# Performance work log

Hardware: AMD Instinct MI355X
Metric: run time of the kernel (lower is better)

The kernel has to match this reference:

```python
import jax, jax.numpy as jnp
import numpy as np

EPS = 1e-06


def euler_xyz_to_mat(e):
    # scipy Rotation.from_euler('xyz', [a,b,c]) is extrinsic: R = Rz(c) @ Ry(b) @ Rx(a)
    a, b, c = e[..., 0], e[..., 1], e[..., 2]
    sa, ca = jnp.sin(a), jnp.cos(a)
    sb, cb = jnp.sin(b), jnp.cos(b)
    sc, cc = jnp.sin(c), jnp.cos(c)
    r00 = cc * cb
    r01 = cc * sb * sa - sc * ca
    r02 = cc * sb * ca + sc * sa
    r10 = sc * cb
    r11 = sc * sb * sa + cc * ca
    r12 = sc * sb * ca - cc * sa
    r20 = -sb
    r21 = cb * sa
    r22 = cb * ca
    R = jnp.stack([r00, r01, r02, r10, r11, r12, r20, r21, r22], axis=-1)
    return R.reshape(e.shape[:-1] + (3, 3))


def to_transform(positions, orientations):
    # positions, orientations: [B, S, 3] -> poses [B, S, 4, 4]
    R = euler_xyz_to_mat(orientations)
    top = jnp.concatenate([R, positions[..., None]], axis=-1)  # [B,S,3,4]
    bottom = jnp.broadcast_to(
        jnp.array([0.0, 0.0, 0.0, 1.0], dtype=positions.dtype),
        positions.shape[:2] + (1, 4))
    return jnp.concatenate([top, bottom], axis=-2)


def odometry_to_track(poses):
    # cumulative left-product along seq: track[0]=I, track[i]=track[i-1] @ poses[:, i]
    B = poses.shape[0]
    eye = jnp.broadcast_to(jnp.eye(4, dtype=poses.dtype), (B, 1, 4, 4))
    shifted = jnp.concatenate([eye, poses[:, 1:]], axis=1)
    return jax.lax.associative_scan(
        lambda x, y: jnp.einsum('bsij,bsjk->bsik', x, y), shifted, axis=1)


def rotation_loss(rot1, rot2):
    # geodesic angle between rotations via trace of R1 @ R2^T
    R = jnp.einsum('bsij,bskj->bsik', rot1, rot2)
    cos = (R[:, :, 0, 0] + R[:, :, 1, 1] + R[:, :, 2, 2] - 1.0) / 2.0
    cos = jnp.clip(cos, -1.0 + EPS, 1.0 - EPS)
    return jnp.mean(jnp.arccos(cos))


def setup_inputs() -> dict:
    key = jax.random.key(0)
    k1, k2, k3 = jax.random.split(key, 3)
    B, S = 64, 4096
    return {
        'y_hat': jax.random.normal(k1, (B, S, 6), dtype=jnp.float32),
        'gt_positions': jax.random.normal(k2, (B, S, 3), dtype=jnp.float32),
        'gt_orientations': jax.random.normal(k3, (B, S, 3), dtype=jnp.float32),
    }


def reference(y_hat, gt_positions, gt_orientations):
    alphas = (1.0, 1.0)
    betas = (1.0, 1.0)
    gammas = (0.5, 0.5)

    pred_ori = y_hat[:, :, :3]
    pred_pos = y_hat[:, :, 3:]

    # ---- odometry loss ----
    mse_pos = jnp.mean((pred_pos - gt_positions) ** 2)
    mae_pos = jnp.mean(jnp.abs(pred_pos - gt_positions))
    pose_est = to_transform(pred_pos, pred_ori)
    pose_gt = to_transform(gt_positions, gt_orientations)
    odom_rot = rotation_loss(pose_est[:, :, :3, :3], pose_gt[:, :, :3, :3])
    odom_loss = alphas[0] * odom_rot + alphas[1] * (mse_pos + mae_pos)

    # ---- trajectory loss ----
    traj_gt = odometry_to_track(pose_gt)
    traj_est = odometry_to_track(pose_est)
    t_gt = traj_gt[:, :, :3, 3]
    t_est = traj_est[:, :, :3, 3]
    traj_mse = jnp.mean((t_est - t_gt) ** 2)
    traj_mae = jnp.mean(jnp.abs(t_est - t_gt))
    traj_rot = rotation_loss(traj_est[:, :, :3, :3], traj_gt[:, :, :3, :3])
    traj_loss = betas[0] * traj_rot + betas[1] * (traj_mse + traj_mae)

    return gammas[0] * odom_loss + gammas[1] * traj_loss
```

## Files before the change

kernel.cpp:

```cpp
#include <hip/hip_runtime.h>
#include <math.h>

#define NB 64
#define NS 4096
#define SEGS 8
#define TPB 256
#define CHUNK 2
#define STEPS (NS / SEGS)
#define NWAVES (TPB / 64)
#define NSEGB (NB * SEGS)
#define K3_TPB 512
#define K3_W (K3_TPB / 64)
#define FTPB 512

#define FB_T 512
#define FB_CHUNK (NS / FB_T)
#define FB_W (FB_T / 64)

struct Q {
  float w, x, y, z;
};
struct QT {
  Q q;
  float tx, ty, tz;
};

__device__ __forceinline__ Q qmul(const Q &a, const Q &b) {
  Q c;
  c.w = a.w * b.w - a.x * b.x - a.y * b.y - a.z * b.z;
  c.x = a.w * b.x + b.w * a.x + a.y * b.z - a.z * b.y;
  c.y = a.w * b.y + b.w * a.y + a.z * b.x - a.x * b.z;
  c.z = a.w * b.z + b.w * a.z + a.x * b.y - a.y * b.x;
  return c;
}

__device__ __forceinline__ Q qconj(const Q &q) {
  Q c;
  c.w = q.w;
  c.x = -q.x;
  c.y = -q.y;
  c.z = -q.z;
  return c;
}

__device__ __forceinline__ void qrot(const Q &q, float vx, float vy, float vz,
                                     float &ox, float &oy, float &oz) {
  const float tx = 2.f * (q.y * vz - q.z * vy);
  const float ty = 2.f * (q.z * vx - q.x * vz);
  const float tz = 2.f * (q.x * vy - q.y * vx);
  ox = vx + q.w * tx + (q.y * tz - q.z * ty);
  oy = vy + q.w * ty + (q.z * tx - q.x * tz);
  oz = vz + q.w * tz + (q.x * ty - q.y * tx);
}

__device__ __forceinline__ void qt_id(QT &x) {
  x.q.w = 1.f;
  x.q.x = x.q.y = x.q.z = 0.f;
  x.tx = x.ty = x.tz = 0.f;
}

__device__ __forceinline__ QT qt_mul(const QT &a, const QT &b) {
  QT c;
  c.q = qmul(a.q, b.q);
  float rx, ry, rz;
  qrot(a.q, b.tx, b.ty, b.tz, rx, ry, rz);
  c.tx = rx + a.tx;
  c.ty = ry + a.ty;
  c.tz = rz + a.tz;
  return c;
}

__device__ __forceinline__ QT qt_shfl_up(const QT &v, int delta) {
  QT y;
  y.q.w = __shfl_up(v.q.w, delta, 64);
  y.q.x = __shfl_up(v.q.x, delta, 64);
  y.q.y = __shfl_up(v.q.y, delta, 64);
  y.q.z = __shfl_up(v.q.z, delta, 64);
  y.tx = __shfl_up(v.tx, delta, 64);
  y.ty = __shfl_up(v.ty, delta, 64);
  y.tz = __shfl_up(v.tz, delta, 64);
  return y;
}

__device__ __forceinline__ float fast_acosf(float x) {
  const float ax = fabsf(x);
  float p = fmaf(ax, -0.0187293f, 0.0742610f);
  p = fmaf(p, ax, -0.2121144f);
  p = fmaf(p, ax, 1.5707288f);
  const float r = sqrtf(fmaxf(1.f - ax, 0.f)) * p;
  return (x >= 0.f) ? r : (3.14159274f - r);
}

__device__ __forceinline__ float angle_from_cos(float cosv) {
  cosv = fminf(fmaxf(cosv, -1.f + 1e-6f), 1.f - 1e-6f);
  return fast_acosf(cosv);
}

__device__ __forceinline__ Q euler_to_quat(float a, float b, float c) {
  float sa, ca, sb, cb, sc, cc;
  __sincosf(0.5f * a, &sa, &ca);
  __sincosf(0.5f * b, &sb, &cb);
  __sincosf(0.5f * c, &sc, &cc);
  Q q;
  q.w = cc * cb * ca + sc * sb * sa;
  q.x = cc * cb * sa - sc * sb * ca;
  q.y = cc * sb * ca + sc * cb * sa;
  q.z = sc * cb * ca - cc * sb * sa;
  return q;
}

__device__ __forceinline__ void block_reduce3_store(float v0, float v1,
                                                    float v2,
                                                    float *__restrict__ dst,
                                                    int lane, int wave,
                                                    int tid, int nwaves) {
#pragma unroll
  for (int o = 32; o > 0; o >>= 1) {
    v0 += __shfl_xor(v0, o, 64);
    v1 += __shfl_xor(v1, o, 64);
    v2 += __shfl_xor(v2, o, 64);
  }
  __shared__ float red[8][3];
  if (lane == 0) {
    red[wave][0] = v0;
    red[wave][1] = v1;
    red[wave][2] = v2;
  }
  __syncthreads();
  if (tid == 0) {
    float a = 0.f, b = 0.f, c = 0.f;
    for (int w = 0; w < nwaves; ++w) {
      a += red[w][0];
      b += red[w][1];
      c += red[w][2];
    }
    dst[0] = a;
    dst[1] = b;
    dst[2] = c;
  }
}


__global__ __launch_bounds__(TPB) void k1_scan(
    const float *__restrict__ y_hat, const float *__restrict__ gt_pos,
    const float *__restrict__ gt_ori, float *__restrict__ wsl,
    float *__restrict__ aggs, float *__restrict__ part1) {
  const int blk = blockIdx.x;
  const int b = blk >> 3;
  const int seg = blk & (SEGS - 1);
  const int tid = threadIdx.x;
  const int lane = tid & 63;
  const int wave = tid >> 6;
  const int s0 = seg * STEPS + tid * CHUNK;

  float s_sq = 0.f, s_abs = 0.f, s_rot = 0.f;

  QT P1e, P1g, P2e, P2g;
  {
    const float *y6 = y_hat + ((size_t)b * NS + s0) * 6;
    const float *g3 = gt_pos + ((size_t)b * NS + s0) * 3;
    const float *o3 = gt_ori + ((size_t)b * NS + s0) * 3;
    const float px = y6[3], py = y6[4], pz = y6[5];
    const float gx = g3[0], gy = g3[1], gz = g3[2];
    P1e.q = euler_to_quat(y6[0], y6[1], y6[2]);
    P1e.tx = px; P1e.ty = py; P1e.tz = pz;
    P1g.q = euler_to_quat(o3[0], o3[1], o3[2]);
    P1g.tx = gx; P1g.ty = gy; P1g.tz = gz;
    const float dx = px - gx, dy = py - gy, dz = pz - gz;
    s_sq += dx * dx + dy * dy + dz * dz;
    s_abs += fabsf(dx) + fabsf(dy) + fabsf(dz);
    const float d = P1e.q.w * P1g.q.w + P1e.q.x * P1g.q.x +
                    P1e.q.y * P1g.q.y + P1e.q.z * P1g.q.z;
    s_rot += angle_from_cos(2.f * d * d - 1.f);
    if (s0 == 0) {
      qt_id(P1e);
      qt_id(P1g);
    }
  }
  {
    const int s1 = s0 + 1;
    const float *y6 = y_hat + ((size_t)b * NS + s1) * 6;
    const float *g3 = gt_pos + ((size_t)b * NS + s1) * 3;
    const float *o3 = gt_ori + ((size_t)b * NS + s1) * 3;
    const float px = y6[3], py = y6[4], pz = y6[5];
    const float gx = g3[0], gy = g3[1], gz = g3[2];
    P2e.q = euler_to_quat(y6[0], y6[1], y6[2]);
    P2e.tx = px; P2e.ty = py; P2e.tz = pz;
    P2g.q = euler_to_quat(o3[0], o3[1], o3[2]);
    P2g.tx = gx; P2g.ty = gy; P2g.tz = gz;
    const float dx = px - gx, dy = py - gy, dz = pz - gz;
    s_sq += dx * dx + dy * dy + dz * dz;
    s_abs += fabsf(dx) + fabsf(dy) + fabsf(dz);
    const float d = P2e.q.w * P2g.q.w + P2e.q.x * P2g.q.x +
                    P2e.q.y * P2g.q.y + P2e.q.z * P2g.q.z;
    s_rot += angle_from_cos(2.f * d * d - 1.f);
  }

  QT Ie = qt_mul(P1e, P2e);
  QT Ig = qt_mul(P1g, P2g);
#pragma unroll
  for (int o = 1; o < 64; o <<= 1) {
    QT pe = qt_shfl_up(Ie, o);
    QT pg = qt_shfl_up(Ig, o);
    if (lane >= o) {
      Ie = qt_mul(pe, Ie);
      Ig = qt_mul(pg, Ig);
    }
  }

  QT Ee = qt_shfl_up(Ie, 1);
  QT Eg = qt_shfl_up(Ig, 1);
  if (lane == 0) {
    qt_id(Ee);
    qt_id(Eg);
  }

  __shared__ float aggE[NWAVES][8];
  __shared__ float aggG[NWAVES][8];
  if (lane == 63) {
    aggE[wave][0] = Ie.q.w; aggE[wave][1] = Ie.q.x;
    aggE[wave][2] = Ie.q.y; aggE[wave][3] = Ie.q.z;
    aggE[wave][4] = Ie.tx; aggE[wave][5] = Ie.ty; aggE[wave][6] = Ie.tz;
    aggG[wave][0] = Ig.q.w; aggG[wave][1] = Ig.q.x;
    aggG[wave][2] = Ig.q.y; aggG[wave][3] = Ig.q.z;
    aggG[wave][4] = Ig.tx; aggG[wave][5] = Ig.ty; aggG[wave][6] = Ig.tz;
  }
  __syncthreads();

  QT We, Wg;
  qt_id(We);
  qt_id(Wg);
  for (int w = 0; w < wave; ++w) {
    QT ae, ag;
    ae.q.w = aggE[w][0]; ae.q.x = aggE[w][1];
    ae.q.y = aggE[w][2]; ae.q.z = aggE[w][3];
    ae.tx = aggE[w][4]; ae.ty = aggE[w][5]; ae.tz = aggE[w][6];
    ag.q.w = aggG[w][0]; ag.q.x = aggG[w][1];
    ag.q.y = aggG[w][2]; ag.q.z = aggG[w][3];
    ag.tx = aggG[w][4]; ag.ty = aggG[w][5]; ag.tz = aggG[w][6];
    We = qt_mul(We, ae);
    Wg = qt_mul(Wg, ag);
  }

  QT Be = qt_mul(We, Ee);
  QT Bg = qt_mul(Wg, Eg);

  QT L1e = qt_mul(Be, P1e);
  QT L1g = qt_mul(Bg, P1g);
  QT L2e = qt_mul(L1e, P2e);
  QT L2g = qt_mul(L1g, P2g);

  float4 *q4 = (float4 *)(wsl + (size_t)b * 10 * NS);
  float4 *lt4 = q4 + NS;
  float2 *g2 = (float2 *)(lt4 + NS);
  {
    const Q qm = qmul(L1e.q, qconj(L1g.q));
    q4[s0] = make_float4(qm.w, qm.x, qm.y, qm.z);
    lt4[s0] = make_float4(L1e.tx, L1e.ty, L1e.tz, L1g.tx);
    g2[s0] = make_float2(L1g.ty, L1g.tz);
  }
  {
    const Q qm = qmul(L2e.q, qconj(L2g.q));
    q4[s0 + 1] = make_float4(qm.w, qm.x, qm.y, qm.z);
    lt4[s0 + 1] = make_float4(L2e.tx, L2e.ty, L2e.tz, L2g.tx);
    g2[s0 + 1] = make_float2(L2g.ty, L2g.tz);
  }

  if (tid == TPB - 1) {
    float *ag = aggs + (size_t)blk * 16;
    ag[0] = L2e.q.w; ag[1] = L2e.q.x; ag[2] = L2e.q.y; ag[3] = L2e.q.z;
    ag[4] = L2e.tx; ag[5] = L2e.ty; ag[6] = L2e.tz;
    ag[8] = L2g.q.w; ag[9] = L2g.q.x; ag[10] = L2g.q.y; ag[11] = L2g.q.z;
    ag[12] = L2g.tx; ag[13] = L2g.ty; ag[14] = L2g.tz;
  }

  block_reduce3_store(s_sq, s_abs, s_rot, part1 + (size_t)blk * 3, lane, wave,
                      tid, NWAVES);
}

__global__ __launch_bounds__(K3_TPB) void k3_traj(const float *__restrict__ wsl,
                                                  const float *__restrict__ aggs,
                                                  float *__restrict__ part2) {
  const int blk = blockIdx.x;
  const int b = blk >> 3;
  const int seg = blk & (SEGS - 1);
  const int tid = threadIdx.x;
  const int lane = tid & 63;
  const int wave = tid >> 6;
  const int s = seg * STEPS + tid;

  QT Ee, Eg;
  qt_id(Ee);
  qt_id(Eg);
  const float *abase = aggs + (size_t)(b * SEGS) * 16;
  for (int w = 0; w < seg; ++w) {
    const float *ag = abase + (size_t)w * 16;
    QT ae, agm;
    ae.q.w = ag[0]; ae.q.x = ag[1]; ae.q.y = ag[2]; ae.q.z = ag[3];
    ae.tx = ag[4]; ae.ty = ag[5]; ae.tz = ag[6];
    agm.q.w = ag[8]; agm.q.x = ag[9]; agm.q.y = ag[10]; agm.q.z = ag[11];
    agm.tx = ag[12]; agm.ty = ag[13]; agm.tz = ag[14];
    Ee = qt_mul(Ee, ae);
    Eg = qt_mul(Eg, agm);
  }

  const Q u = qmul(qconj(Eg.q), Ee.q);
  const float dt0x = Ee.tx - Eg.tx;
  const float dt0y = Ee.ty - Eg.ty;
  const float dt0z = Ee.tz - Eg.tz;

  const float4 *q4 = (const float4 *)(wsl + (size_t)b * 10 * NS);
  const float4 *lt4 = q4 + NS;
  const float2 *g2 = (const float2 *)(lt4 + NS);
  const float4 qm = q4[s];
  const float4 lt = lt4[s];
  const float2 gv = g2[s];

  const float wdot = u.w * qm.x - u.x * qm.y - u.y * qm.z - u.z * qm.w;
  (void)wdot;
  const float mw = qm.x, mx = qm.y, my = qm.z, mz = qm.w;
  const float wd = u.w * mw - u.x * mx - u.y * my - u.z * mz;
  float s_rot = angle_from_cos(2.f * wd * wd - 1.f);

  float ux, uy, uz, vx, vy, vz;
  qrot(Ee.q, lt.x, lt.y, lt.z, ux, uy, uz);
  qrot(Eg.q, lt.w, gv.x, gv.y, vx, vy, vz);
  const float dx = ux - vx + dt0x;
  const float dy = uy - vy + dt0y;
  const float dz = uz - vz + dt0z;

  float s_sq = dx * dx + dy * dy + dz * dz;
  float s_abs = fabsf(dx) + fabsf(dy) + fabsf(dz);

  block_reduce3_store(s_sq, s_abs, s_rot, part2 + (size_t)blk * 3, lane, wave,
                      tid, K3_W);
}

__global__ __launch_bounds__(FTPB) void finalize_parts(
    const float *__restrict__ part1, const float *__restrict__ part2,
    float *__restrict__ out) {
  const int tid = threadIdx.x;
  const int lane = tid & 63;
  const int wave = tid >> 6;

  float v[6];
#pragma unroll
  for (int k = 0; k < 3; ++k) {
    v[k] = part1[(size_t)tid * 3 + k];
    v[3 + k] = part2[(size_t)tid * 3 + k];
  }
#pragma unroll
  for (int o = 32; o > 0; o >>= 1) {
#pragma unroll
    for (int k = 0; k < 6; ++k) v[k] += __shfl_xor(v[k], o, 64);
  }
  __shared__ float red[FTPB / 64][6];
  if (lane == 0) {
#pragma unroll
    for (int k = 0; k < 6; ++k) red[wave][k] = v[k];
  }
  __syncthreads();
  if (tid == 0) {
    double a[6];
#pragma unroll
    for (int k = 0; k < 6; ++k) {
      double t = 0.0;
#pragma unroll
      for (int w = 0; w < FTPB / 64; ++w) t += (double)red[w][k];
      a[k] = t;
    }
    const double n3 = (double)NB * (double)NS * 3.0;
    const double n1 = (double)NB * (double)NS;
    const double odom = a[2] / n1 + (a[0] / n3 + a[1] / n3);
    const double traj = a[5] / n1 + (a[3] / n3 + a[4] / n3);
    out[0] = (float)(0.5 * odom + 0.5 * traj);
  }
}

struct SE3 {
  float r[9];
  float t[3];
};

__device__ __forceinline__ void se3_id(SE3 &x) {
#pragma unroll
  for (int i = 0; i < 9; ++i) x.r[i] = 0.f;
  x.r[0] = x.r[4] = x.r[8] = 1.f;
  x.t[0] = x.t[1] = x.t[2] = 0.f;
}

__device__ __forceinline__ SE3 se3_mul(const SE3 &a, const SE3 &b) {
  SE3 c;
#pragma unroll
  for (int i = 0; i < 3; ++i) {
#pragma unroll
    for (int j = 0; j < 3; ++j) {
      c.r[i * 3 + j] = fmaf(a.r[i * 3 + 0], b.r[0 * 3 + j],
                       fmaf(a.r[i * 3 + 1], b.r[1 * 3 + j],
                            a.r[i * 3 + 2] * b.r[2 * 3 + j]));
    }
    c.t[i] = fmaf(a.r[i * 3 + 0], b.t[0],
             fmaf(a.r[i * 3 + 1], b.t[1],
             fmaf(a.r[i * 3 + 2], b.t[2], a.t[i])));
  }
  return c;
}

__device__ __forceinline__ SE3 build_pose(float a, float b, float c,
                                          float tx, float ty, float tz) {
  float sa, ca, sb, cb, sc, cc;
  __sincosf(a, &sa, &ca);
  __sincosf(b, &sb, &cb);
  __sincosf(c, &sc, &cc);
  SE3 p;
  p.r[0] = cc * cb;
  p.r[1] = cc * sb * sa - sc * ca;
  p.r[2] = cc * sb * ca + sc * sa;
  p.r[3] = sc * cb;
  p.r[4] = sc * sb * sa + cc * ca;
  p.r[5] = sc * sb * ca - cc * sa;
  p.r[6] = -sb;
  p.r[7] = cb * sa;
  p.r[8] = cb * ca;
  p.t[0] = tx;
  p.t[1] = ty;
  p.t[2] = tz;
  return p;
}

__device__ __forceinline__ SE3 se3_shfl_up(const SE3 &x, int delta) {
  SE3 y;
#pragma unroll
  for (int i = 0; i < 9; ++i) y.r[i] = __shfl_up(x.r[i], delta, 64);
#pragma unroll
  for (int i = 0; i < 3; ++i) y.t[i] = __shfl_up(x.t[i], delta, 64);
  return y;
}

__device__ __forceinline__ float geo_angle(const SE3 &A, const SE3 &B) {
  float dot = 0.f;
#pragma unroll
  for (int k = 0; k < 9; ++k) dot = fmaf(A.r[k], B.r[k], dot);
  return angle_from_cos(0.5f * (dot - 1.f));
}

__global__ __launch_bounds__(FB_T) void traj_loss_main(
    const float *__restrict__ y_hat, const float *__restrict__ gt_pos,
    const float *__restrict__ gt_ori, double *__restrict__ acc) {
  const int b = blockIdx.x;
  const int tid = threadIdx.x;
  const int lane = tid & 63;
  const int wave = tid >> 6;
  const int s0 = tid * FB_CHUNK;

  const float *yb = y_hat + (size_t)b * NS * 6;
  const float *gp = gt_pos + (size_t)b * NS * 3;
  const float *go = gt_ori + (size_t)b * NS * 3;

  float s_sq_pos = 0.f, s_abs_pos = 0.f, s_rot_odom = 0.f;

  SE3 Le, Lg;
  se3_id(Le);
  se3_id(Lg);

  for (int i = 0; i < FB_CHUNK; ++i) {
    const int s = s0 + i;
    const float *y6 = yb + (size_t)s * 6;
    const float *g3 = gp + (size_t)s * 3;
    const float *o3 = go + (size_t)s * 3;
    const float px = y6[3], py = y6[4], pz = y6[5];
    const float gx = g3[0], gy = g3[1], gz = g3[2];

    SE3 Pe = build_pose(y6[0], y6[1], y6[2], px, py, pz);
    SE3 Pg = build_pose(o3[0], o3[1], o3[2], gx, gy, gz);

    const float dx = px - gx, dy = py - gy, dz = pz - gz;
    s_sq_pos += dx * dx + dy * dy + dz * dz;
    s_abs_pos += fabsf(dx) + fabsf(dy) + fabsf(dz);
    s_rot_odom += geo_angle(Pe, Pg);

    if (s != 0) {
      Le = se3_mul(Le, Pe);
      Lg = se3_mul(Lg, Pg);
    }
  }

  SE3 Ie = Le, Ig = Lg;
#pragma unroll
  for (int o = 1; o < 64; o <<= 1) {
    SE3 pe = se3_shfl_up(Ie, o);
    SE3 pg = se3_shfl_up(Ig, o);
    if (lane >= o) {
      Ie = se3_mul(pe, Ie);
      Ig = se3_mul(pg, Ig);
    }
  }

  __shared__ float aggE[FB_W][12];
  __shared__ float aggG[FB_W][12];
  if (lane == 63) {
#pragma unroll
    for (int k = 0; k < 9; ++k) {
      aggE[wave][k] = Ie.r[k];
      aggG[wave][k] = Ig.r[k];
    }
#pragma unroll
    for (int k = 0; k < 3; ++k) {
      aggE[wave][9 + k] = Ie.t[k];
      aggG[wave][9 + k] = Ig.t[k];
    }
  }
  __syncthreads();

  SE3 Te, Tg;
  se3_id(Te);
  se3_id(Tg);
  for (int w = 0; w < wave; ++w) {
    SE3 ae, ag;
#pragma unroll
    for (int k = 0; k < 9; ++k) {
      ae.r[k] = aggE[w][k];
      ag.r[k] = aggG[w][k];
    }
#pragma unroll
    for (int k = 0; k < 3; ++k) {
      ae.t[k] = aggE[w][9 + k];
      ag.t[k] = aggG[w][9 + k];
    }
    Te = se3_mul(Te, ae);
    Tg = se3_mul(Tg, ag);
  }

  SE3 Ee = se3_shfl_up(Ie, 1);
  SE3 Eg = se3_shfl_up(Ig, 1);
  if (lane == 0) {
    se3_id(Ee);
    se3_id(Eg);
  }
  Te = se3_mul(Te, Ee);
  Tg = se3_mul(Tg, Eg);

  float s_sq_tr = 0.f, s_abs_tr = 0.f, s_rot_tr = 0.f;
  for (int i = 0; i < FB_CHUNK; ++i) {
    const int s = s0 + i;
    const float *y6 = yb + (size_t)s * 6;
    const float *g3 = gp + (size_t)s * 3;
    const float *o3 = go + (size_t)s * 3;
    if (s != 0) {
      SE3 Pe = build_pose(y6[0], y6[1], y6[2], y6[3], y6[4], y6[5]);
      SE3 Pg = build_pose(o3[0], o3[1], o3[2], g3[0], g3[1], g3[2]);
      Te = se3_mul(Te, Pe);
      Tg = se3_mul(Tg, Pg);
    }
    const float dx = Te.t[0] - Tg.t[0];
    const float dy = Te.t[1] - Tg.t[1];
    const float dz = Te.t[2] - Tg.t[2];
    s_sq_tr += dx * dx + dy * dy + dz * dz;
    s_abs_tr += fabsf(dx) + fabsf(dy) + fabsf(dz);
    s_rot_tr += geo_angle(Te, Tg);
  }

#pragma unroll
  for (int o = 32; o > 0; o >>= 1) {
    s_sq_pos += __shfl_xor(s_sq_pos, o, 64);
    s_abs_pos += __shfl_xor(s_abs_pos, o, 64);
    s_rot_odom += __shfl_xor(s_rot_odom, o, 64);
    s_sq_tr += __shfl_xor(s_sq_tr, o, 64);
    s_abs_tr += __shfl_xor(s_abs_tr, o, 64);
    s_rot_tr += __shfl_xor(s_rot_tr, o, 64);
  }
  if (lane == 0) {
    atomicAdd(&acc[0], (double)s_sq_pos);
    atomicAdd(&acc[1], (double)s_abs_pos);
    atomicAdd(&acc[2], (double)s_rot_odom);
    atomicAdd(&acc[3], (double)s_sq_tr);
    atomicAdd(&acc[4], (double)s_abs_tr);
    atomicAdd(&acc[5], (double)s_rot_tr);
  }
}

__global__ void init_acc(double *acc) {
  const int i = threadIdx.x;
  if (i < 6) acc[i] = 0.0;
}

__global__ void finalize_acc(const double *__restrict__ acc,
                             float *__restrict__ out) {
  const double n3 = (double)NB * (double)NS * 3.0;
  const double n1 = (double)NB * (double)NS;
  const double odom = acc[2] / n1 + (acc[0] / n3 + acc[1] / n3);
  const double traj = acc[5] / n1 + (acc[3] / n3 + acc[4] / n3);
  out[0] = (float)(0.5 * odom + 0.5 * traj);
}

extern "C" void kernel_launch(void *const *d_in, const int *in_sizes, int n_in,
                              void *d_out, int out_size, void *d_ws,
                              size_t ws_size, hipStream_t stream) {
  const float *y_hat = (const float *)d_in[0];
  const float *gt_pos = (const float *)d_in[1];
  const float *gt_ori = (const float *)d_in[2];

  float *wsl = (float *)d_ws;
  const size_t wsl_elems = (size_t)NB * 10 * NS;
  float *aggs = wsl + wsl_elems;
  float *part1 = aggs + (size_t)NSEGB * 16;
  float *part2 = part1 + (size_t)NSEGB * 3;
  const size_t need = (wsl_elems + (size_t)NSEGB * 22) * sizeof(float);

  if (ws_size >= need) {
    k1_scan<<<NSEGB, TPB, 0, stream>>>(y_hat, gt_pos, gt_ori, wsl, aggs,
                                       part1);
    k3_traj<<<NSEGB, K3_TPB, 0, stream>>>(wsl, aggs, part2);
    finalize_parts<<<1, FTPB, 0, stream>>>(part1, part2, (float *)d_out);
  } else {
    double *acc = (double *)d_ws;
    init_acc<<<1, 64, 0, stream>>>(acc);
    traj_loss_main<<<NB, FB_T, 0, stream>>>(y_hat, gt_pos, gt_ori, acc);
    finalize_acc<<<1, 1, 0, stream>>>(acc, (float *)d_out);
  }
}
```

Measured before the change: 24.73 us.

## Split wave scan into quaternion and translation scans, store relative quaternion in fp16

The intra-wave scan over rigid transforms is split into two passes. The first is a quaternion-only scan. The second rotates each lane's translation by the exclusive quaternion prefix and runs a plain additive prefix sum, which cuts the shuffle count and arithmetic per scan step. The relative quaternion stored to workspace is packed as four fp16 values instead of four fp32, reducing workspace traffic from 10 to 8 floats per element. This risks precision loss in the trajectory rotation angle, since the acos near cos≈1 is sensitive to quaternion error.

```diff
diff --git a/kernel.cpp b/kernel.cpp
--- a/kernel.cpp
+++ b/kernel.cpp
@@ -1,4 +1,5 @@
 #include <hip/hip_runtime.h>
+#include <hip/hip_fp16.h>
 #include <math.h>
 
 #define NB 64
@@ -53,9 +54,13 @@
   oz = vz + q.w * tz + (q.x * ty - q.y * tx);
 }
 
+__device__ __forceinline__ void q_id(Q &q) {
+  q.w = 1.f;
+  q.x = q.y = q.z = 0.f;
+}
+
 __device__ __forceinline__ void qt_id(QT &x) {
-  x.q.w = 1.f;
-  x.q.x = x.q.y = x.q.z = 0.f;
+  q_id(x.q);
   x.tx = x.ty = x.tz = 0.f;
 }
 
@@ -70,15 +75,12 @@
   return c;
 }
 
-__device__ __forceinline__ QT qt_shfl_up(const QT &v, int delta) {
-  QT y;
-  y.q.w = __shfl_up(v.q.w, delta, 64);
-  y.q.x = __shfl_up(v.q.x, delta, 64);
-  y.q.y = __shfl_up(v.q.y, delta, 64);
-  y.q.z = __shfl_up(v.q.z, delta, 64);
-  y.tx = __shfl_up(v.tx, delta, 64);
-  y.ty = __shfl_up(v.ty, delta, 64);
-  y.tz = __shfl_up(v.tz, delta, 64);
+__device__ __forceinline__ Q q_shfl_up(const Q &v, int delta) {
+  Q y;
+  y.w = __shfl_up(v.w, delta, 64);
+  y.x = __shfl_up(v.x, delta, 64);
+  y.y = __shfl_up(v.y, delta, 64);
+  y.z = __shfl_up(v.z, delta, 64);
   return y;
 }
 
@@ -196,34 +198,72 @@
     s_rot += angle_from_cos(2.f * d * d - 1.f);
   }
 
-  QT Ie = qt_mul(P1e, P2e);
-  QT Ig = qt_mul(P1g, P2g);
+  Q Aqe = qmul(P1e.q, P2e.q);
+  Q Aqg = qmul(P1g.q, P2g.q);
+  float tAex, tAey, tAez, tAgx, tAgy, tAgz;
+  {
+    float rx, ry, rz;
+    qrot(P1e.q, P2e.tx, P2e.ty, P2e.tz, rx, ry, rz);
+    tAex = P1e.tx + rx; tAey = P1e.ty + ry; tAez = P1e.tz + rz;
+    qrot(P1g.q, P2g.tx, P2g.ty, P2g.tz, rx, ry, rz);
+    tAgx = P1g.tx + rx; tAgy = P1g.ty + ry; tAgz = P1g.tz + rz;
+  }
+
+  Q Iqe = Aqe, Iqg = Aqg;
 #pragma unroll
   for (int o = 1; o < 64; o <<= 1) {
-    QT pe = qt_shfl_up(Ie, o);
-    QT pg = qt_shfl_up(Ig, o);
+    Q pe = q_shfl_up(Iqe, o);
+    Q pg = q_shfl_up(Iqg, o);
     if (lane >= o) {
-      Ie = qt_mul(pe, Ie);
-      Ig = qt_mul(pg, Ig);
-    }
-  }
-
-  QT Ee = qt_shfl_up(Ie, 1);
-  QT Eg = qt_shfl_up(Ig, 1);
+      Iqe = qmul(pe, Iqe);
+      Iqg = qmul(pg, Iqg);
+    }
+  }
+
+  Q Eqe = q_shfl_up(Iqe, 1);
+  Q Eqg = q_shfl_up(Iqg, 1);
   if (lane == 0) {
-    qt_id(Ee);
-    qt_id(Eg);
+    q_id(Eqe);
+    q_id(Eqg);
+  }
+
+  float vex, vey, vez, vgx, vgy, vgz;
+  qrot(Eqe, tAex, tAey, tAez, vex, vey, vez);
+  qrot(Eqg, tAgx, tAgy, tAgz, vgx, vgy, vgz);
+#pragma unroll
+  for (int o = 1; o < 64; o <<= 1) {
+    const float a0 = __shfl_up(vex, o, 64);
+    const float a1 = __shfl_up(vey, o, 64);
+    const float a2 = __shfl_up(vez, o, 64);
+    const float b0 = __shfl_up(vgx, o, 64);
+    const float b1 = __shfl_up(vgy, o, 64);
+    const float b2 = __shfl_up(vgz, o, 64);
+    if (lane >= o) {
+      vex += a0; vey += a1; vez += a2;
+      vgx += b0; vgy += b1; vgz += b2;
+    }
+  }
+
+  float Etex = __shfl_up(vex, 1, 64);
+  float Etey = __shfl_up(vey, 1, 64);
+  float Etez = __shfl_up(vez, 1, 64);
+  float Etgx = __shfl_up(vgx, 1, 64);
+  float Etgy = __shfl_up(vgy, 1, 64);
+  float Etgz = __shfl_up(vgz, 1, 64);
+  if (lane == 0) {
+    Etex = Etey = Etez = 0.f;
+    Etgx = Etgy = Etgz = 0.f;
   }
 
   __shared__ float aggE[NWAVES][8];
   __shared__ float aggG[NWAVES][8];
   if (lane == 63) {
-    aggE[wave][0] = Ie.q.w; aggE[wave][1] = Ie.q.x;
-    aggE[wave][2] = Ie.q.y; aggE[wave][3] = Ie.q.z;
-    aggE[wave][4] = Ie.tx; aggE[wave][5] = Ie.ty; aggE[wave][6] = Ie.tz;
-    aggG[wave][0] = Ig.q.w; aggG[wave][1] = Ig.q.x;
-    aggG[wave][2] = Ig.q.y; aggG[wave][3] = Ig.q.z;
-    aggG[wave][4] = Ig.tx; aggG[wave][5] = Ig.ty; aggG[wave][6] = Ig.tz;
+    aggE[wave][0] = Iqe.w; aggE[wave][1] = Iqe.x;
+    aggE[wave][2] = Iqe.y; aggE[wave][3] = Iqe.z;
+    aggE[wave][4] = vex; aggE[wave][5] = vey; aggE[wave][6] = vez;
+    aggG[wave][0] = Iqg.w; aggG[wave][1] = Iqg.x;
+    aggG[wave][2] = Iqg.y; aggG[wave][3] = Iqg.z;
+    aggG[wave][4] = vgx; aggG[wave][5] = vgy; aggG[wave][6] = vgz;
   }
   __syncthreads();
 
@@ -242,6 +282,9 @@
     Wg = qt_mul(Wg, ag);
   }
 
+  QT Ee, Eg;
+  Ee.q = Eqe; Ee.tx = Etex; Ee.ty = Etey; Ee.tz = Etez;
+  Eg.q = Eqg; Eg.tx = Etgx; Eg.ty = Etgy; Eg.tz = Etgz;
   QT Be = qt_mul(We, Ee);
   QT Bg = qt_mul(Wg, Eg);
 
@@ -250,18 +293,25 @@
   QT L2e = qt_mul(L1e, P2e);
   QT L2g = qt_mul(L1g, P2g);
 
-  float4 *q4 = (float4 *)(wsl + (size_t)b * 10 * NS);
-  float4 *lt4 = q4 + NS;
-  float2 *g2 = (float2 *)(lt4 + NS);
+  float *base = wsl + (size_t)b * 8 * NS;
+  float2 *q2 = (float2 *)base;
+  float4 *lt4 = (float4 *)(base + (size_t)2 * NS);
+  float2 *g2 = (float2 *)(base + (size_t)6 * NS);
   {
     const Q qm = qmul(L1e.q, qconj(L1g.q));
-    q4[s0] = make_float4(qm.w, qm.x, qm.y, qm.z);
+    union { __half2 h[2]; float2 f; } pk;
+    pk.h[0] = __floats2half2_rn(qm.w, qm.x);
+    pk.h[1] = __floats2half2_rn(qm.y, qm.z);
+    q2[s0] = pk.f;
     lt4[s0] = make_float4(L1e.tx, L1e.ty, L1e.tz, L1g.tx);
     g2[s0] = make_float2(L1g.ty, L1g.tz);
   }
   {
     const Q qm = qmul(L2e.q, qconj(L2g.q));
-    q4[s0 + 1] = make_float4(qm.w, qm.x, qm.y, qm.z);
+    union { __half2 h[2]; float2 f; } pk;
+    pk.h[0] = __floats2half2_rn(qm.w, qm.x);
+    pk.h[1] = __floats2half2_rn(qm.y, qm.z);
+    q2[s0 + 1] = pk.f;
     lt4[s0 + 1] = make_float4(L2e.tx, L2e.ty, L2e.tz, L2g.tx);
     g2[s0 + 1] = make_float2(L2g.ty, L2g.tz);
   }
@@ -309,16 +359,20 @@
   const float dt0y = Ee.ty - Eg.ty;
   const float dt0z = Ee.tz - Eg.tz;
 
-  const float4 *q4 = (const float4 *)(wsl + (size_t)b * 10 * NS);
-  const float4 *lt4 = q4 + NS;
-  const float2 *g2 = (const float2 *)(lt4 + NS);
-  const float4 qm = q4[s];
+  const float *base = wsl + (size_t)b * 8 * NS;
+  const float2 *q2 = (const float2 *)base;
+  const float4 *lt4 = (const float4 *)(base + (size_t)2 * NS);
+  const float2 *g2 = (const float2 *)(base + (size_t)6 * NS);
+
+  union { float2 f; __half2 h[2]; } pk;
+  pk.f = q2[s];
+  const float2 wx = __half22float2(pk.h[0]);
+  const float2 yz = __half22float2(pk.h[1]);
+  const float mw = wx.x, mx = wx.y, my = yz.x, mz = yz.y;
+
   const float4 lt = lt4[s];
   const float2 gv = g2[s];
 
-  const float wdot = u.w * qm.x - u.x * qm.y - u.y * qm.z - u.z * qm.w;
-  (void)wdot;
-  const float mw = qm.x, mx = qm.y, my = qm.z, mz = qm.w;
   const float wd = u.w * mw - u.x * mx - u.y * my - u.z * mz;
   float s_rot = angle_from_cos(2.f * wd * wd - 1.f);
 
@@ -601,7 +655,7 @@
   const float *gt_ori = (const float *)d_in[2];
 
   float *wsl = (float *)d_ws;
-  const size_t wsl_elems = (size_t)NB * 10 * NS;
+  const size_t wsl_elems = (size_t)NB * 8 * NS;
   float *aggs = wsl + wsl_elems;
   float *part1 = aggs + (size_t)NSEGB * 16;
   float *part2 = part1 + (size_t)NSEGB * 3;
```

Result: faster. 24.21 us (-2.1%).
